# Kernel optimization log

Measured on AMD Instinct MI355X. Metric: run time of the kernel, lower is better.

## Reference

```python
import jax, jax.numpy as jnp
import numpy as np

EPS = 1e-6

def _rms_norm(t, g):
    # t: [B, S, C] (applied before the view to heads, matching the torch code)
    y = t.astype(jnp.float32)
    y = jax.lax.rsqrt(jnp.mean(y * y, axis=-1, keepdims=True) + EPS)
    return (t * y * g).astype(t.dtype)

def _apply_rope(t, cos, sin):
    # t: [B, S, N, D]; cos/sin: [1, S, 1, D//2]; interleaved pair rotation
    b, s, n, d = t.shape
    tr = t.reshape(b, s, n, d // 2, 2)
    tre, tim = tr[..., 0], tr[..., 1]
    out = jnp.stack([tre * cos - tim * sin, tre * sin + tim * cos], axis=-1)
    return out.reshape(b, s, n, d)

def setup_inputs() -> dict:
    key = jax.random.key(0)
    ks = jax.random.split(key, 8)
    B, S, DIM, N, D = 2, 1024, 3072, 24, 128
    x = jax.random.normal(ks[0], (B, S, DIM), dtype=jnp.float32)
    seq_lens = jax.random.randint(ks[1], (B,), S // 2, S + 1, dtype=jnp.int32)
    grid_sizes = jnp.tile(jnp.array([[16, 8, 8]], dtype=jnp.int32), (B, 1))
    # rope angle table [1024, D//2]: pos * inv_freq
    inv_freq = 1.0 / (10000.0 ** (jnp.arange(D // 2, dtype=jnp.float32) * 2.0 / D))
    freqs = jnp.arange(1024, dtype=jnp.float32)[:, None] * inv_freq[None, :]
    sc = 1.0 / np.sqrt(DIM)
    Wq = jax.random.normal(ks[2], (DIM, DIM), dtype=jnp.float32) * sc
    Wk = jax.random.normal(ks[3], (DIM, DIM), dtype=jnp.float32) * sc
    Wv = jax.random.normal(ks[4], (DIM, DIM), dtype=jnp.float32) * sc
    Wo = jax.random.normal(ks[5], (DIM, DIM), dtype=jnp.float32) * sc
    bq = jnp.zeros((DIM,), jnp.float32); bk = jnp.zeros((DIM,), jnp.float32)
    bv = jnp.zeros((DIM,), jnp.float32); bo = jnp.zeros((DIM,), jnp.float32)
    gq = jnp.ones((DIM,), jnp.float32); gk = jnp.ones((DIM,), jnp.float32)
    return {"x": x, "seq_lens": seq_lens, "grid_sizes": grid_sizes, "freqs": freqs,
            "Wq": Wq, "bq": bq, "Wk": Wk, "bk": bk, "Wv": Wv, "bv": bv,
            "Wo": Wo, "bo": bo, "gq": gq, "gk": gk}

def reference(x, seq_lens, grid_sizes, freqs, Wq, bq, Wk, bk, Wv, bv, Wo, bo, gq, gk):
    b, s, dim = x.shape
    d = 2 * freqs.shape[1]          # head_dim
    n = dim // d                    # num_heads
    q = _rms_norm(x @ Wq.T + bq, gq).reshape(b, s, n, d)
    k = _rms_norm(x @ Wk.T + bk, gk).reshape(b, s, n, d)
    v = (x @ Wv.T + bv).reshape(b, s, n, d)
    ang = freqs[:s]                 # [S, D//2]
    cos = jnp.cos(ang)[None, :, None, :]
    sin = jnp.sin(ang)[None, :, None, :]
    q = _apply_rope(q, cos, sin)
    k = _apply_rope(k, cos, sin)
    # full attention (window_size = (-1,-1)), varlen key masking via seq_lens
    scale = d ** -0.5
    scores = jnp.einsum('bind,bjnd->bnij', q, k) * scale   # [B,N,S,S]
    key_valid = jnp.arange(s)[None, :] < seq_lens[:, None]  # [B,S]
    scores = jnp.where(key_valid[:, None, None, :], scores, jnp.finfo(scores.dtype).min)
    p = jax.nn.softmax(scores, axis=-1)
    out = jnp.einsum('bnij,bjnd->bind', p, v).reshape(b, s, dim)
    return out @ Wo.T + bo
```

## Files before the change

### kernel.cpp

```cpp
#include <hip/hip_runtime.h>
#include <cmath>

#define BB   2
#define SS   1024
#define DIMM 3072
#define NHH  24
#define HDD  128
#define MM   (BB * SS)

typedef _Float16 f16;
typedef __attribute__((ext_vector_type(8))) _Float16 half8;
typedef __attribute__((ext_vector_type(4))) float floatx4;
typedef unsigned int u32;
typedef const __attribute__((address_space(1))) u32* gp1;
typedef __attribute__((address_space(3))) u32* lp3;

__device__ __forceinline__ void gload_lds16(const void* g, void* l) {
    __builtin_amdgcn_global_load_lds((gp1)g, (lp3)l, 16, 0, 0);
}

__global__ __launch_bounds__(256) void cvt_f16_kernel(
    const float* __restrict__ in, f16* __restrict__ outp, int n8)
{
    int i = blockIdx.x * 256 + threadIdx.x;
    if (i >= n8) return;
    const float4* p = (const float4*)(in + (size_t)i * 8);
    float4 a = p[0], b = p[1];
    half8 h = {(f16)a.x, (f16)a.y, (f16)a.z, (f16)a.w,
               (f16)b.x, (f16)b.y, (f16)b.z, (f16)b.w};
    *(half8*)(outp + (size_t)i * 8) = h;
}

template<bool QKV>
__global__ __launch_bounds__(256) void gemm_f16(
    const f16* __restrict__ A,
    const float* __restrict__ W0, const float* __restrict__ W1, const float* __restrict__ W2,
    const float* __restrict__ b0, const float* __restrict__ b1, const float* __restrict__ b2,
    f16* __restrict__ D0, f16* __restrict__ D1, f16* __restrict__ D2,
    float* __restrict__ F)
{
    constexpr int K = DIMM;
    constexpr int NSTEP = K / 32;
    constexpr int TS = 128 * 32;
    __shared__ __align__(16) f16 As[4 * TS];
    __shared__ __align__(16) f16 Bs[2 * TS];

    const int tid  = threadIdx.x;
    const int lane = tid & 63;
    const int wave = tid >> 6;
    const int wm = wave >> 1, wn = wave & 1;
    const int lr = lane & 15;
    const int lq = lane >> 4;

    const int id  = blockIdx.x;
    const int cpx = (int)gridDim.x >> 3;
    const int swz = (id & 7) * cpx + (id >> 3);
    const int bm = (swz & 15) << 7;
    const int bn = (swz >> 4) << 7;

    const float* W; const float* bias; f16* D = nullptr;
    int nloc = bn;
    if constexpr (QKV) {
        int sel = bn / DIMM;
        nloc = bn - sel * DIMM;
        W    = sel == 0 ? W0 : (sel == 1 ? W1 : W2);
        bias = sel == 0 ? b0 : (sel == 1 ? b1 : b2);
        D    = sel == 0 ? D0 : (sel == 1 ? D1 : D2);
    } else { W = W0; bias = b0; }

    const int r0 = tid >> 2;
    const int c8 = (tid & 3) << 3;
    const float* bp0 = W + (size_t)(nloc + r0) * K + c8;
    const float* bp1 = W + (size_t)(nloc + r0 + 64) * K + c8;

    const int arow_l = lane >> 2;
    const int acol_l = (lane & 3) << 3;
    const f16* agbase = A + (size_t)bm * K;

    float4 sA[4], sB[4];
    auto LOADB = [&](int t, float4* s) {
        const int k0 = t * 32;
        s[0] = *(const float4*)(bp0 + k0); s[1] = *(const float4*)(bp0 + k0 + 4);
        s[2] = *(const float4*)(bp1 + k0); s[3] = *(const float4*)(bp1 + k0 + 4);
    };
    auto STOREB = [&](f16* Bbuf, const float4* s) {
        half8 h0 = {(f16)s[0].x, (f16)s[0].y, (f16)s[0].z, (f16)s[0].w,
                    (f16)s[1].x, (f16)s[1].y, (f16)s[1].z, (f16)s[1].w};
        half8 h1 = {(f16)s[2].x, (f16)s[2].y, (f16)s[2].z, (f16)s[2].w,
                    (f16)s[3].x, (f16)s[3].y, (f16)s[3].z, (f16)s[3].w};
        *(half8*)&Bbuf[r0 * 32 + c8]        = h0;
        *(half8*)&Bbuf[(r0 + 64) * 32 + c8] = h1;
    };
    auto STAGEA = [&](int t, int buf) {
        const int k0 = t * 32;
#pragma unroll
        for (int i = 0; i < 2; ++i) {
            int rbase = wave * 32 + i * 16;
            gload_lds16(agbase + (size_t)(rbase + arow_l) * K + k0 + acol_l,
                        &As[buf * TS + rbase * 32]);
        }
    };

    floatx4 acc[4][4];
#pragma unroll
    for (int i = 0; i < 4; ++i)
#pragma unroll
        for (int j = 0; j < 4; ++j) acc[i][j] = (floatx4){0.f, 0.f, 0.f, 0.f};

    auto COMPUTE = [&](const f16* Ac, const f16* Bc) {
        half8 af[4], bf[4];
#pragma unroll
        for (int i = 0; i < 4; ++i) {
            af[i] = *(const half8*)&Ac[(wm * 64 + i * 16 + lr) * 32 + lq * 8];
            bf[i] = *(const half8*)&Bc[(wn * 64 + i * 16 + lr) * 32 + lq * 8];
        }
        __builtin_amdgcn_s_setprio(1);
#pragma unroll
        for (int mi = 0; mi < 4; ++mi)
#pragma unroll
            for (int ni = 0; ni < 4; ++ni)
                acc[mi][ni] = __builtin_amdgcn_mfma_f32_16x16x32_f16(af[mi], bf[ni], acc[mi][ni], 0, 0, 0);
        __builtin_amdgcn_s_setprio(0);
    };

    LOADB(0, sA);
    STAGEA(0, 0);
    LOADB(1, sB);
    STAGEA(1, 1);
    STOREB(&Bs[0], sA);
    asm volatile("s_waitcnt vmcnt(6)" ::: "memory");
    asm volatile("s_waitcnt lgkmcnt(0)" ::: "memory");
    __builtin_amdgcn_s_barrier();

    for (int ks = 0; ks < NSTEP; ks += 2) {
        if (ks + 2 < NSTEP) { LOADB(ks + 2, sA); STAGEA(ks + 2, (ks + 2) & 3); }
        asm volatile("s_waitcnt vmcnt(12)" ::: "memory");
        __builtin_amdgcn_s_barrier();
        STOREB(&Bs[TS], sB);
        COMPUTE(&As[(ks & 3) * TS], &Bs[0]);
        asm volatile("s_waitcnt lgkmcnt(0)" ::: "memory");

        if (ks + 3 < NSTEP) { LOADB(ks + 3, sB); STAGEA(ks + 3, (ks + 3) & 3); }
        asm volatile("s_waitcnt vmcnt(12)" ::: "memory");
        __builtin_amdgcn_s_barrier();
        if (ks + 2 < NSTEP) STOREB(&Bs[0], sA);
        COMPUTE(&As[((ks + 1) & 3) * TS], &Bs[TS]);
        asm volatile("s_waitcnt lgkmcnt(0)" ::: "memory");
    }

    const int crow0 = bm + wm * 64 + (lq << 2);
    const int ccol0 = nloc + wn * 64;
#pragma unroll
    for (int ni = 0; ni < 4; ++ni) {
        const int col = ccol0 + ni * 16 + lr;
        const float bv = bias[col];
#pragma unroll
        for (int mi = 0; mi < 4; ++mi) {
            const int row = crow0 + mi * 16;
#pragma unroll
            for (int r2 = 0; r2 < 4; ++r2) {
                if constexpr (QKV)
                    D[(size_t)(row + r2) * DIMM + col] = (f16)(acc[mi][ni][r2] + bv);
                else
                    F[(size_t)(row + r2) * DIMM + col] = acc[mi][ni][r2] + bv;
            }
        }
    }
}

__global__ __launch_bounds__(192) void rmsnorm_rope_f16(
    f16* __restrict__ q, f16* __restrict__ k,
    const float* __restrict__ gq, const float* __restrict__ gk,
    const float* __restrict__ freqs)
{
    f16* t = (blockIdx.y == 0) ? q : k;
    const float* g = (blockIdx.y == 0) ? gq : gk;
    const int row = blockIdx.x;
    const int s = row & (SS - 1);
    const int tid = threadIdx.x;
    f16* base = t + (size_t)row * DIMM + tid * 16;

    half8 v0 = *(const half8*)base;
    half8 v1 = *(const half8*)(base + 8);
    float v[16];
#pragma unroll
    for (int j = 0; j < 8; ++j) { v[j] = (float)v0[j]; v[8 + j] = (float)v1[j]; }

    float ssq = 0.f;
#pragma unroll
    for (int j = 0; j < 16; ++j) ssq += v[j] * v[j];
#pragma unroll
    for (int off = 32; off > 0; off >>= 1) ssq += __shfl_down(ssq, off, 64);
    __shared__ float red[3];
    if ((tid & 63) == 0) red[tid >> 6] = ssq;
    __syncthreads();
    float tot = red[0] + red[1] + red[2];
    float sc = rsqrtf(tot * (1.0f / (float)DIMM) + 1e-6f);

    const float* gp = g + tid * 16;
    float y[16];
#pragma unroll
    for (int j = 0; j < 16; ++j) y[j] = v[j] * sc * gp[j];

#pragma unroll
    for (int p = 0; p < 8; ++p) {
        int idx = tid * 16 + 2 * p;
        int f = (idx & 127) >> 1;
        float ang = freqs[s * 64 + f];
        float cc = cosf(ang), sn = sinf(ang);
        float e = y[2 * p], o = y[2 * p + 1];
        y[2 * p]     = e * cc - o * sn;
        y[2 * p + 1] = e * sn + o * cc;
    }
    half8 o0, o1;
#pragma unroll
    for (int j = 0; j < 8; ++j) { o0[j] = (f16)y[j]; o1[j] = (f16)y[8 + j]; }
    *(half8*)base       = o0;
    *(half8*)(base + 8) = o1;
}

__global__ __launch_bounds__(256) void flash_attn_f16(
    const f16* __restrict__ Q, const f16* __restrict__ K,
    const f16* __restrict__ V, const int* __restrict__ seq_lens,
    f16* __restrict__ O)
{
    __shared__ __align__(16) f16 QPs[64 * 128];
    __shared__ __align__(16) f16 Ks[64 * 128];
    __shared__ __align__(16) f16 Vt[128 * 64];

    const int tid  = threadIdx.x;
    const int lane = tid & 63;
    const int wave = tid >> 6;
    const int ln = lane & 15;
    const int lq = lane >> 4;
    const int i0 = blockIdx.x * 64;
    const int h  = blockIdx.y;
    const int b  = blockIdx.z;
    const int slen = seq_lens[b];
    const float scale = 0.08838834764831845f;
    const size_t gstride = NHH * HDD;

    const f16* Qg = Q + ((size_t)(b * SS + i0) * NHH + h) * HDD;
#pragma unroll
    for (int rep = 0; rep < 4; ++rep) {
        int u = tid + rep * 256;
        int r = u >> 4, d0 = (u & 15) << 3;
        half8 qv = *(const half8*)(Qg + (size_t)r * gstride + d0);
        *(half8*)(QPs + r * 128 + (d0 ^ ((r & 7) << 3))) = qv;
    }
    __syncthreads();

    half8 qfrag[4];
    {
        int rq = wave * 16 + ln;
#pragma unroll
        for (int ks = 0; ks < 4; ++ks)
            qfrag[ks] = *(const half8*)(QPs + rq * 128 + ((ks * 32 + lq * 8) ^ ((rq & 7) << 3)));
    }

    floatx4 accO[8];
#pragma unroll
    for (int dt = 0; dt < 8; ++dt) accO[dt] = (floatx4){0.f, 0.f, 0.f, 0.f};
    float mrow[4] = {-3.0e38f, -3.0e38f, -3.0e38f, -3.0e38f};
    float lrow[4] = {0.f, 0.f, 0.f, 0.f};

    const int nT = (slen + 63) >> 6;
    for (int t = 0; t < nT; ++t) {
        const int j0g = t * 64;
        __syncthreads();

        const f16* Kg = K + ((size_t)(b * SS + j0g) * NHH + h) * HDD;
#pragma unroll
        for (int rep = 0; rep < 4; ++rep) {
            int u = tid + rep * 256;
            int r = u >> 4, d0 = (u & 15) << 3;
            half8 kv = *(const half8*)(Kg + (size_t)r * gstride + d0);
            *(half8*)(Ks + r * 128 + (d0 ^ ((r & 7) << 3))) = kv;
        }
        const f16* Vg = V + ((size_t)(b * SS + j0g) * NHH + h) * HDD;
#pragma unroll
        for (int rep = 0; rep < 2; ++rep) {
            int u = tid + rep * 256;
            int jp = u & 31, j0 = jp * 2;
            int d0 = (u >> 5) << 3;
            half8 va = *(const half8*)(Vg + (size_t)j0 * gstride + d0);
            half8 vb = *(const half8*)(Vg + (size_t)(j0 + 1) * gstride + d0);
#pragma unroll
            for (int i = 0; i < 8; ++i) {
                int d = d0 + i;
                union { f16 h[2]; u32 w; } pk;
                pk.h[0] = va[i]; pk.h[1] = vb[i];
                *(u32*)(Vt + d * 64 + (j0 ^ ((d & 7) << 3))) = pk.w;
            }
        }
        __syncthreads();

        floatx4 acc_s[4];
#pragma unroll
        for (int nt = 0; nt < 4; ++nt) {
            acc_s[nt] = (floatx4){0.f, 0.f, 0.f, 0.f};
            int rk = nt * 16 + ln;
#pragma unroll
            for (int ks = 0; ks < 4; ++ks) {
                half8 kf = *(const half8*)(Ks + rk * 128 + ((ks * 32 + lq * 8) ^ ((rk & 7) << 3)));
                acc_s[nt] = __builtin_amdgcn_mfma_f32_16x16x32_f16(qfrag[ks], kf, acc_s[nt], 0, 0, 0);
            }
        }

        float s[4][4];
#pragma unroll
        for (int nt = 0; nt < 4; ++nt) {
            int j = j0g + nt * 16 + ln;
            bool valid = (j < slen);
#pragma unroll
            for (int r = 0; r < 4; ++r)
                s[nt][r] = valid ? acc_s[nt][r] * scale : -3.0e38f;
        }
        float fct[4];
#pragma unroll
        for (int r = 0; r < 4; ++r) {
            float m4 = fmaxf(fmaxf(s[0][r], s[1][r]), fmaxf(s[2][r], s[3][r]));
            m4 = fmaxf(m4, __shfl_xor(m4, 1, 64));
            m4 = fmaxf(m4, __shfl_xor(m4, 2, 64));
            m4 = fmaxf(m4, __shfl_xor(m4, 4, 64));
            m4 = fmaxf(m4, __shfl_xor(m4, 8, 64));
            float mn = fmaxf(mrow[r], m4);
            fct[r] = __expf(mrow[r] - mn);
            mrow[r] = mn;
            float ls = 0.f;
#pragma unroll
            for (int nt = 0; nt < 4; ++nt) {
                float p = __expf(s[nt][r] - mn);
                s[nt][r] = p;
                ls += p;
            }
            ls += __shfl_xor(ls, 1, 64);
            ls += __shfl_xor(ls, 2, 64);
            ls += __shfl_xor(ls, 4, 64);
            ls += __shfl_xor(ls, 8, 64);
            lrow[r] = lrow[r] * fct[r] + ls;
        }

#pragma unroll
        for (int nt = 0; nt < 4; ++nt) {
#pragma unroll
            for (int r = 0; r < 4; ++r) {
                int rw = lq * 4 + r;
                int j = nt * 16 + ln;
                QPs[(wave * 16 + rw) * 128 + (j ^ ((rw & 7) << 3))] = (f16)s[nt][r];
            }
        }

#pragma unroll
        for (int dt = 0; dt < 8; ++dt)
#pragma unroll
            for (int r = 0; r < 4; ++r) accO[dt][r] *= fct[r];

        half8 pfrag[2];
#pragma unroll
        for (int js = 0; js < 2; ++js)
            pfrag[js] = *(const half8*)(QPs + (wave * 16 + ln) * 128 + ((js * 32 + lq * 8) ^ ((ln & 7) << 3)));
#pragma unroll
        for (int dt = 0; dt < 8; ++dt) {
            int d = dt * 16 + ln;
#pragma unroll
            for (int js = 0; js < 2; ++js) {
                half8 vf = *(const half8*)(Vt + d * 64 + ((js * 32 + lq * 8) ^ ((d & 7) << 3)));
                accO[dt] = __builtin_amdgcn_mfma_f32_16x16x32_f16(pfrag[js], vf, accO[dt], 0, 0, 0);
            }
        }
    }

    float linv[4];
#pragma unroll
    for (int r = 0; r < 4; ++r) linv[r] = 1.0f / lrow[r];
    f16* Og = O + ((size_t)(b * SS + i0) * NHH + h) * HDD;
#pragma unroll
    for (int dt = 0; dt < 8; ++dt) {
#pragma unroll
        for (int r = 0; r < 4; ++r) {
            int qr = wave * 16 + lq * 4 + r;
            int d = dt * 16 + ln;
            Og[(size_t)qr * gstride + d] = (f16)(accO[dt][r] * linv[r]);
        }
    }
}

extern "C" void kernel_launch(void* const* d_in, const int* in_sizes, int n_in,
                              void* d_out, int out_size, void* d_ws, size_t ws_size,
                              hipStream_t stream)
{
    const float* x     = (const float*)d_in[0];
    const int*   seq   = (const int*)d_in[1];
    const float* freqs = (const float*)d_in[3];
    const float* Wq    = (const float*)d_in[4];
    const float* bq    = (const float*)d_in[5];
    const float* Wk    = (const float*)d_in[6];
    const float* bk    = (const float*)d_in[7];
    const float* Wv    = (const float*)d_in[8];
    const float* bv    = (const float*)d_in[9];
    const float* Wo    = (const float*)d_in[10];
    const float* bo    = (const float*)d_in[11];
    const float* gq    = (const float*)d_in[12];
    const float* gk    = (const float*)d_in[13];

    float* out = (float*)d_out;
    const size_t MD = (size_t)MM * DIMM;

    f16* X16 = (f16*)d_ws;
    f16* q16 = X16 + MD;
    f16* k16 = X16 + 2 * MD;
    f16* v16 = (f16*)d_out;

    cvt_f16_kernel<<<(int)(MD / (256 * 8)), 256, 0, stream>>>(x, X16, (int)(MD / 8));
    gemm_f16<true><<<(MM / 128) * (3 * DIMM / 128), 256, 0, stream>>>(
        X16, Wq, Wk, Wv, bq, bk, bv, q16, k16, v16, nullptr);
    rmsnorm_rope_f16<<<dim3(MM, 2), 192, 0, stream>>>(q16, k16, gq, gk, freqs);
    flash_attn_f16<<<dim3(SS / 64, NHH, BB), 256, 0, stream>>>(q16, k16, v16, seq, X16);
    gemm_f16<false><<<(MM / 128) * (DIMM / 128), 256, 0, stream>>>(
        X16, Wo, nullptr, nullptr, bo, nullptr, nullptr, nullptr, nullptr, nullptr, out);
}
```

Measured before the change: 353.7 us.

## Deepen GEMM B-operand register prefetch to three stages with four-way unrolled loop

The fp32 weight tiles are now prefetched into registers three k-steps ahead using four rotating register sets, instead of two. The main loop is unrolled by four, and the fp16 store of B into LDS moves after the MFMA compute so it overlaps with it. The aim is to hide more global-load latency for the B operand. The extra register sets raise VGPR pressure, and the hand-tuned vmcnt waits must still match the new count of loads in flight.

Result: slower. 405.5 us (+14.7%).

```diff
diff --git a/kernel.cpp b/kernel.cpp
--- a/kernel.cpp
+++ b/kernel.cpp
@@ -77,7 +77,7 @@
     const int acol_l = (lane & 3) << 3;
     const f16* agbase = A + (size_t)bm * K;
 
-    float4 sA[4], sB[4];
+    float4 s0[4], s1[4], s2[4], s3[4];
     auto LOADB = [&](int t, float4* s) {
         const int k0 = t * 32;
         s[0] = *(const float4*)(bp0 + k0); s[1] = *(const float4*)(bp0 + k0 + 4);
@@ -123,30 +123,32 @@
         __builtin_amdgcn_s_setprio(0);
     };
 
-    LOADB(0, sA);
-    STAGEA(0, 0);
-    LOADB(1, sB);
-    STAGEA(1, 1);
-    STOREB(&Bs[0], sA);
-    asm volatile("s_waitcnt vmcnt(6)" ::: "memory");
+    LOADB(0, s0); LOADB(1, s1); LOADB(2, s2);
+    STAGEA(0, 0); STAGEA(1, 1);
+    asm volatile("s_waitcnt vmcnt(12)" ::: "memory");
+    STOREB(&Bs[0], s0);
+    asm volatile("s_waitcnt vmcnt(2)" ::: "memory");
     asm volatile("s_waitcnt lgkmcnt(0)" ::: "memory");
     __builtin_amdgcn_s_barrier();
 
-    for (int ks = 0; ks < NSTEP; ks += 2) {
-        if (ks + 2 < NSTEP) { LOADB(ks + 2, sA); STAGEA(ks + 2, (ks + 2) & 3); }
-        asm volatile("s_waitcnt vmcnt(12)" ::: "memory");
-        __builtin_amdgcn_s_barrier();
-        STOREB(&Bs[TS], sB);
-        COMPUTE(&As[(ks & 3) * TS], &Bs[0]);
-        asm volatile("s_waitcnt lgkmcnt(0)" ::: "memory");
-
-        if (ks + 3 < NSTEP) { LOADB(ks + 3, sB); STAGEA(ks + 3, (ks + 3) & 3); }
-        asm volatile("s_waitcnt vmcnt(12)" ::: "memory");
-        __builtin_amdgcn_s_barrier();
-        if (ks + 2 < NSTEP) STOREB(&Bs[0], sA);
-        COMPUTE(&As[((ks + 1) & 3) * TS], &Bs[TS]);
-        asm volatile("s_waitcnt lgkmcnt(0)" ::: "memory");
-    }
+#define SUBITER(P, SLD, SST)                                                     \
+    {                                                                            \
+        if (ks + (P) + 3 < NSTEP) LOADB(ks + (P) + 3, SLD);                      \
+        if (ks + (P) + 2 < NSTEP) STAGEA(ks + (P) + 2, ((P) + 2) & 3);           \
+        asm volatile("s_waitcnt vmcnt(12)" ::: "memory");                        \
+        __builtin_amdgcn_s_barrier();                                            \
+        COMPUTE(&As[((P) & 3) * TS], &Bs[((P) & 1) * TS]);                       \
+        if (ks + (P) + 1 < NSTEP) STOREB(&Bs[(((P) + 1) & 1) * TS], SST);        \
+        asm volatile("s_waitcnt lgkmcnt(0)" ::: "memory");                       \
+    }
+
+    for (int ks = 0; ks < NSTEP; ks += 4) {
+        SUBITER(0, s3, s1)
+        SUBITER(1, s0, s2)
+        SUBITER(2, s1, s3)
+        SUBITER(3, s2, s0)
+    }
+#undef SUBITER
 
     const int crow0 = bm + wm * 64 + (lq << 2);
     const int ccol0 = nloc + wn * 64;
```
